# Kernel optimization log

Measured on AMD Instinct MI355X. Metric: run time of the kernel, lower is better.

Reference implementation:

```python
import jax, jax.numpy as jnp
import numpy as np

QK_C = 64
VX_C = 128

def conv1x1(x, W, b):
    # x: [B,C,H,W], W: [O,C], b: [O] -> [B,O,H,W]
    return jnp.einsum('bchw,oc->bohw', x, W) + b[None, :, None, None]

def setup_inputs() -> dict:
    key = jax.random.key(0)
    ks = jax.random.split(key, 9)
    B, H, W = 4, 64, 64
    x = jax.random.normal(ks[0], (B, QK_C, H, W), dtype=jnp.float32)
    x_h = jax.random.normal(ks[1], (B, VX_C, H, W), dtype=jnp.float32)
    qc = QK_C // 4
    s_qk = 1.0 / np.sqrt(QK_C)
    s_v = 1.0 / np.sqrt(VX_C)
    Wq = jax.random.normal(ks[2], (qc, QK_C), dtype=jnp.float32) * s_qk
    bq = jax.random.normal(ks[3], (qc,), dtype=jnp.float32) * 0.01
    Wk = jax.random.normal(ks[4], (qc, QK_C), dtype=jnp.float32) * s_qk
    bk = jax.random.normal(ks[5], (qc,), dtype=jnp.float32) * 0.01
    Wv = jax.random.normal(ks[6], (VX_C, VX_C), dtype=jnp.float32) * s_v
    bv = jax.random.normal(ks[7], (VX_C,), dtype=jnp.float32) * 0.01
    # gamma initialized to zero in the torch module; use a small nonzero value
    # so the attention branch actually contributes to the output/gradients.
    gamma = jnp.array([0.1], dtype=jnp.float32)
    return {"x": x, "x_h": x_h, "Wq": Wq, "bq": bq, "Wk": Wk, "bk": bk,
            "Wv": Wv, "bv": bv, "gamma": gamma}

def reference(x, x_h, Wq, bq, Wk, bk, Wv, bv, gamma):
    B, C, H, W = x_h.shape
    b, c, h, w = x.shape
    N = h * w
    # 1x1-conv projections, flattened over spatial positions
    q = conv1x1(x, Wq, bq).reshape(b, -1, N)          # [B, qc, N]
    k = conv1x1(x, Wk, bk).reshape(b, -1, N)          # [B, qc, N]
    v = conv1x1(x_h, Wv, bv).reshape(B, C, H * W)     # [B, C, N]
    # energy[b, i, j] = <q[:, i], k[:, j]>
    energy = jnp.einsum('bdi,bdj->bij', q, k)          # [B, N, N]
    attention = jax.nn.softmax(energy, axis=-1)
    # out[b, c, i] = sum_j v[b, c, j] * attention[b, i, j]
    out = jnp.einsum('bcj,bij->bci', v, attention)     # [B, C, N]
    out = out.reshape(B, C, H, W)
    return gamma[0] * out + x_h
```

## Files before the change

### kernel.cpp

```cpp
#include <hip/hip_runtime.h>

#define BB 4
#define NN 4096
#define CQK 64
#define DQ 16
#define CV 128

typedef __attribute__((ext_vector_type(8))) short bf16x8;
typedef __attribute__((ext_vector_type(4))) float f32x4;
typedef __attribute__((ext_vector_type(16))) float f32x16;
typedef __attribute__((ext_vector_type(8))) unsigned short u16x8;
typedef __attribute__((ext_vector_type(4))) unsigned int u32x4;

__device__ __forceinline__ unsigned short f2bf(float f) {
    unsigned int u = __builtin_bit_cast(unsigned int, f);
    u += 0x7FFFu + ((u >> 16) & 1u);
    return (unsigned short)(u >> 16);
}
__device__ __forceinline__ unsigned int pk_trunc(float lo, float hi) {
    unsigned int a = __builtin_bit_cast(unsigned int, lo);
    unsigned int b = __builtin_bit_cast(unsigned int, hi);
    return (a >> 16) | (b & 0xFFFF0000u);
}

__global__ __launch_bounds__(256, 4) void proj(
    const float* __restrict__ x,
    const float* __restrict__ Wq, const float* __restrict__ bq,
    const float* __restrict__ Wk, const float* __restrict__ bk,
    const float* __restrict__ xh,
    const float* __restrict__ Wv, const float* __restrict__ bv,
    unsigned short* __restrict__ qT, unsigned short* __restrict__ kT,
    unsigned short* __restrict__ vB)
{
    __shared__ __align__(16) float smem[8448];
    int tid = threadIdx.x;
    if (blockIdx.x >= 64) {
        float* wvT = smem;
        float* xs  = smem + 4224;
        float* bvs = smem + 8320;
        int bid = blockIdx.x - 64;
        int pt = bid >> 1, h = bid & 1;
        int i0 = pt * 64;
        int b = i0 >> 12, ib = i0 & 4095;
        int co0 = h * 64;
        if (tid < 64) bvs[tid] = bv[co0 + tid];
        int cog = tid & 31, ig = tid >> 5;
        float acc[8][2];
#pragma unroll
        for (int q = 0; q < 8; q++) { acc[q][0] = 0.f; acc[q][1] = 0.f; }

        for (int ch = 0; ch < 2; ch++) {
            for (int t = tid; t < 4096; t += 256) {
                int c = t & 63, col = t >> 6;
                wvT[c * 66 + col] = Wv[(size_t)(co0 + col) * CV + ch * 64 + c];
            }
            for (int t = tid; t < 4096; t += 256) {
                int il = t & 63, c = t >> 6;
                xs[c * 64 + il] = xh[((size_t)b * CV + ch * 64 + c) * NN + ib + il];
            }
            __syncthreads();
            for (int c = 0; c < 64; c++) {
                float2 w2 = *(const float2*)&wvT[c * 66 + cog * 2];
                float4 xa = *(const float4*)&xs[c * 64 + ig * 8];
                float4 xb = *(const float4*)&xs[c * 64 + ig * 8 + 4];
                float xv[8] = { xa.x, xa.y, xa.z, xa.w, xb.x, xb.y, xb.z, xb.w };
#pragma unroll
                for (int q = 0; q < 8; q++) {
                    acc[q][0] += xv[q] * w2.x;
                    acc[q][1] += xv[q] * w2.y;
                }
            }
            __syncthreads();
        }
        int kt = ib >> 6;
        int hb = ig & 1, kc = ig >> 1;
#pragma unroll
        for (int cc = 0; cc < 2; cc++) {
            int co = co0 + cog * 2 + cc;
            int g = co >> 5, cl = co & 31;
            float bb = bvs[cog * 2 + cc];
            u16x8 o;
#pragma unroll
            for (int jj = 0; jj < 8; jj++) o[jj] = f2bf(acc[jj][cc] + bb);
            size_t base = ((size_t)(b * 64 + kt)) * 8192
                        + (size_t)(((g * 4 + kc) * 64 + hb * 32 + cl)) * 8;
            *(u16x8*)(vB + base) = o;
        }
    } else {
        float* wqT = smem;
        float* wkT = smem + 1024;
        float* bqs = smem + 2048;
        float* bks = smem + 2064;
        for (int t = tid; t < 1024; t += 256) {
            int c = t & 63, d = t >> 6;
            wqT[c * 16 + d] = Wq[d * CQK + c];
            wkT[c * 16 + d] = Wk[d * CQK + c];
        }
        if (tid < DQ) { bqs[tid] = bq[tid]; bks[tid] = bk[tid]; }
        __syncthreads();

        int gidx = blockIdx.x * 256 + tid;
        int b = gidx >> 12, i = gidx & 4095;
        float qa[DQ], ka[DQ];
#pragma unroll
        for (int d = 0; d < DQ; d++) { qa[d] = bqs[d]; ka[d] = bks[d]; }
        const float* xp = x + (size_t)b * CQK * NN + i;
        for (int c = 0; c < CQK; c++) {
            float xv = xp[(size_t)c * NN];
            const float4* wq4 = (const float4*)&wqT[c * DQ];
            const float4* wk4 = (const float4*)&wkT[c * DQ];
#pragma unroll
            for (int dd = 0; dd < 4; dd++) {
                float4 a = wq4[dd], e = wk4[dd];
                qa[dd*4+0] += a.x * xv; qa[dd*4+1] += a.y * xv;
                qa[dd*4+2] += a.z * xv; qa[dd*4+3] += a.w * xv;
                ka[dd*4+0] += e.x * xv; ka[dd*4+1] += e.y * xv;
                ka[dd*4+2] += e.z * xv; ka[dd*4+3] += e.w * xv;
            }
        }
        u16x8 q0, q1, k0, k1;
#pragma unroll
        for (int dd = 0; dd < 8; dd++) {
            q0[dd] = f2bf(qa[dd]);     q1[dd] = f2bf(qa[8 + dd]);
            k0[dd] = f2bf(ka[dd]);     k1[dd] = f2bf(ka[8 + dd]);
        }
        u16x8* qo = (u16x8*)(qT + (size_t)gidx * DQ);
        u16x8* ko = (u16x8*)(kT + (size_t)gidx * DQ);
        qo[0] = q0; qo[1] = q1;
        ko[0] = k0; ko[1] = k1;
    }
}

__global__ __launch_bounds__(256, 2) void flash_mfma(
    const unsigned short* __restrict__ qTb,
    const unsigned short* __restrict__ kTb,
    const unsigned short* __restrict__ vB,
    const float* __restrict__ xh,
    const float* __restrict__ gamma,
    float* __restrict__ out)
{
    __shared__ __align__(16) float accs[32 * 132];
    __shared__ float l_s[4 * 2 * 32];

    int tid = threadIdx.x;
    int w = tid >> 6, lane = tid & 63;
    int q32 = lane & 31, half = lane >> 5;
    int b = blockIdx.x >> 7;
    int i0 = (blockIdx.x & 127) * 32;
    f32x16 zf16;
#pragma unroll
    for (int r = 0; r < 16; r++) zf16[r] = 0.f;

    bf16x8 qa = *(const bf16x8*)(qTb + ((size_t)(b * NN + i0 + q32)) * DQ + half * 8);

    f32x16 acc[4];
#pragma unroll
    for (int g = 0; g < 4; g++) acc[g] = zf16;
    float l = 0.f;

    const unsigned short* vtile = vB + ((size_t)(b * 64 + w * 16)) * 8192;
    const unsigned short* kbase = kTb + ((size_t)(b * NN + w * 16 * 64)) * DQ;

    bf16x8 kb[2], vb[16];
#pragma unroll
    for (int mg = 0; mg < 2; mg++)
        kb[mg] = *(const bf16x8*)(kbase + (size_t)(mg * 32 + q32) * DQ + half * 8);
#pragma unroll
    for (int i = 0; i < 16; i++)
        vb[i] = *(const bf16x8*)(vtile + (size_t)i * 512 + (size_t)lane * 8);

    for (int t = 0; t < 16; t++) {
        f32x16 s[2];
        s[0] = __builtin_amdgcn_mfma_f32_32x32x16_bf16(kb[0], qa, zf16, 0, 0, 0);
        s[1] = __builtin_amdgcn_mfma_f32_32x32x16_bf16(kb[1], qa, zf16, 0, 0, 0);
        const unsigned short* ktn = kbase + (size_t)(((t + 1) & 15) * 64) * DQ;
#pragma unroll
        for (int mg = 0; mg < 2; mg++)
            kb[mg] = *(const bf16x8*)(ktn + (size_t)(mg * 32 + q32) * DQ + half * 8);

        const unsigned short* vtn = vtile + ((t < 15) ? 8192 : 0);
#pragma unroll
        for (int u = 0; u < 4; u++) {
            const int mg = u >> 1, h8 = (u & 1) * 8;
            float p0 = __expf(s[mg][h8 + 0]);
            float p1 = __expf(s[mg][h8 + 1]);
            float p2 = __expf(s[mg][h8 + 2]);
            float p3 = __expf(s[mg][h8 + 3]);
            float p4 = __expf(s[mg][h8 + 4]);
            float p5 = __expf(s[mg][h8 + 5]);
            float p6 = __expf(s[mg][h8 + 6]);
            float p7 = __expf(s[mg][h8 + 7]);
            l += ((p0 + p1) + (p2 + p3)) + ((p4 + p5) + (p6 + p7));
            unsigned int A0 = pk_trunc(p0, p1), A1 = pk_trunc(p2, p3);
            unsigned int A2 = pk_trunc(p4, p5), A3 = pk_trunc(p6, p7);
            asm("v_permlane32_swap_b32 %0, %1" : "+v"(A0), "+v"(A2));
            asm("v_permlane32_swap_b32 %0, %1" : "+v"(A1), "+v"(A3));
            u32x4 pbw = { A0, A1, A2, A3 };
            bf16x8 pb = __builtin_bit_cast(bf16x8, pbw);
#pragma unroll
            for (int g = 0; g < 4; g++)
                acc[g] = __builtin_amdgcn_mfma_f32_32x32x16_bf16(vb[g * 4 + u], pb, acc[g], 0, 0, 0);
#pragma unroll
            for (int g = 0; g < 4; g++)
                vb[g * 4 + u] = *(const bf16x8*)(vtn + (size_t)(g * 4 + u) * 512 + (size_t)lane * 8);
        }
        vtile = vtn;
    }

    l_s[(w * 2 + half) * 32 + q32] = l;
    for (int ww = 0; ww < 4; ww++) {
        if (w == ww) {
#pragma unroll
            for (int g = 0; g < 4; g++)
#pragma unroll
                for (int r = 0; r < 4; r++) {
                    float* p = accs + q32 * 132 + g * 32 + r * 8 + half * 4;
                    f32x4 v4 = { acc[g][r*4+0], acc[g][r*4+1], acc[g][r*4+2], acc[g][r*4+3] };
                    if (ww == 0) *(f32x4*)p = v4;
                    else { f32x4 o = *(const f32x4*)p; *(f32x4*)p = o + v4; }
                }
        }
        __syncthreads();
    }

    float gam = gamma[0];
    int q = tid & 31, cg = tid >> 5;
    float L = 0.f;
#pragma unroll
    for (int u = 0; u < 8; u++) L += l_s[u * 32 + q];
    float linv = 1.f / L;
#pragma unroll
    for (int cc = 0; cc < 16; cc++) {
        int c = cg * 16 + cc;
        size_t gi = ((size_t)(b * CV + c)) * NN + i0 + q;
        out[gi] = gam * accs[q * 132 + c] * linv + xh[gi];
    }
}

extern "C" void kernel_launch(void* const* d_in, const int* in_sizes, int n_in,
                              void* d_out, int out_size, void* d_ws, size_t ws_size,
                              hipStream_t stream)
{
    (void)in_sizes; (void)n_in; (void)out_size; (void)ws_size;
    const float* x  = (const float*)d_in[0];
    const float* xh = (const float*)d_in[1];
    const float* Wq = (const float*)d_in[2];
    const float* bq = (const float*)d_in[3];
    const float* Wk = (const float*)d_in[4];
    const float* bk = (const float*)d_in[5];
    const float* Wv = (const float*)d_in[6];
    const float* bv = (const float*)d_in[7];
    const float* gm = (const float*)d_in[8];
    float* out = (float*)d_out;

    char* ws = (char*)d_ws;
    unsigned short* qTb = (unsigned short*)ws;
    unsigned short* kTb = (unsigned short*)(ws + (512 << 10));
    unsigned short* vB  = (unsigned short*)(ws + (1 << 20));

    proj<<<576, 256, 0, stream>>>(x, Wq, bq, Wk, bk, xh, Wv, bv, qTb, kTb, vB);
    flash_mfma<<<BB * 128, 256, 0, stream>>>(qTb, kTb, vB, xh, gm, out);
}
```

Before: 121.3 us.

## Process 64 queries per block with 8 waves sharing V fragments across two query tiles

Each block now handles 64 queries, split into two 32-query tiles, with 512 threads. Each of the 8 waves covers 8 key tiles, and every loaded V fragment feeds MFMAs for both query tiles, which halves V traffic per query. V loads are double-buffered through smaller register sets, and s_setprio is raised around the PV MFMAs. The cross-wave reduction now writes bf16 partials to LDS with one barrier instead of serialized f32 accumulation. This adds bf16 rounding of the partial outputs and uses more LDS, which may lower occupancy.

```diff
diff --git a/kernel.cpp b/kernel.cpp
--- a/kernel.cpp
+++ b/kernel.cpp
@@ -16,6 +16,12 @@
     unsigned int u = __builtin_bit_cast(unsigned int, f);
     u += 0x7FFFu + ((u >> 16) & 1u);
     return (unsigned short)(u >> 16);
+}
+__device__ __forceinline__ unsigned int pk2bf(float a, float b) {
+    return (unsigned int)f2bf(a) | ((unsigned int)f2bf(b) << 16);
+}
+__device__ __forceinline__ float bf2f(unsigned short u) {
+    return __builtin_bit_cast(float, (unsigned int)u << 16);
 }
 __device__ __forceinline__ unsigned int pk_trunc(float lo, float hi) {
     unsigned int a = __builtin_bit_cast(unsigned int, lo);
@@ -131,7 +137,7 @@
     }
 }
 
-__global__ __launch_bounds__(256, 2) void flash_mfma(
+__global__ __launch_bounds__(512, 2) void flash_mfma(
     const unsigned short* __restrict__ qTb,
     const unsigned short* __restrict__ kTb,
     const unsigned short* __restrict__ vB,
@@ -139,101 +145,136 @@
     const float* __restrict__ gamma,
     float* __restrict__ out)
 {
-    __shared__ __align__(16) float accs[32 * 132];
-    __shared__ float l_s[4 * 2 * 32];
+    __shared__ __align__(16) unsigned short part[8 * 64 * 132];
+    __shared__ float l_s[16 * 64];
 
     int tid = threadIdx.x;
     int w = tid >> 6, lane = tid & 63;
     int q32 = lane & 31, half = lane >> 5;
-    int b = blockIdx.x >> 7;
-    int i0 = (blockIdx.x & 127) * 32;
+    int p = blockIdx.x;
+    int b = (p >> 1) & 3;
+    int qg = ((p >> 3) << 1) | (p & 1);
+    int i0 = qg * 64;
     f32x16 zf16;
 #pragma unroll
     for (int r = 0; r < 16; r++) zf16[r] = 0.f;
 
-    bf16x8 qa = *(const bf16x8*)(qTb + ((size_t)(b * NN + i0 + q32)) * DQ + half * 8);
-
-    f32x16 acc[4];
-#pragma unroll
-    for (int g = 0; g < 4; g++) acc[g] = zf16;
-    float l = 0.f;
-
-    const unsigned short* vtile = vB + ((size_t)(b * 64 + w * 16)) * 8192;
-    const unsigned short* kbase = kTb + ((size_t)(b * NN + w * 16 * 64)) * DQ;
-
-    bf16x8 kb[2], vb[16];
+    bf16x8 qaA = *(const bf16x8*)(qTb + ((size_t)(b * NN + i0 + q32)) * DQ + half * 8);
+    bf16x8 qaB = *(const bf16x8*)(qTb + ((size_t)(b * NN + i0 + 32 + q32)) * DQ + half * 8);
+
+    f32x16 accA[4], accB[4];
+#pragma unroll
+    for (int g = 0; g < 4; g++) { accA[g] = zf16; accB[g] = zf16; }
+    float lA = 0.f, lB = 0.f;
+
+    const unsigned short* vtile = vB + ((size_t)(b * 64 + w * 8)) * 8192;
+    const unsigned short* kbase = kTb + ((size_t)(b * NN + w * 8 * 64)) * DQ;
+
+    bf16x8 kb[2], vc0[4], vc1[4];
 #pragma unroll
     for (int mg = 0; mg < 2; mg++)
         kb[mg] = *(const bf16x8*)(kbase + (size_t)(mg * 32 + q32) * DQ + half * 8);
 #pragma unroll
-    for (int i = 0; i < 16; i++)
-        vb[i] = *(const bf16x8*)(vtile + (size_t)i * 512 + (size_t)lane * 8);
-
-    for (int t = 0; t < 16; t++) {
-        f32x16 s[2];
-        s[0] = __builtin_amdgcn_mfma_f32_32x32x16_bf16(kb[0], qa, zf16, 0, 0, 0);
-        s[1] = __builtin_amdgcn_mfma_f32_32x32x16_bf16(kb[1], qa, zf16, 0, 0, 0);
-        const unsigned short* ktn = kbase + (size_t)(((t + 1) & 15) * 64) * DQ;
+    for (int g = 0; g < 4; g++)
+        vc0[g] = *(const bf16x8*)(vtile + (size_t)(g * 4) * 512 + (size_t)lane * 8);
+
+#define PACK_GRP(S0, S1, P, LACC)                                            \
+    _Pragma("unroll")                                                        \
+    for (int u = 0; u < 4; u++) {                                            \
+        const f32x16& sv = (u >> 1) ? (S1) : (S0);                           \
+        const int h8 = (u & 1) * 8;                                          \
+        float p0 = __expf(sv[h8 + 0]), p1 = __expf(sv[h8 + 1]);              \
+        float p2 = __expf(sv[h8 + 2]), p3 = __expf(sv[h8 + 3]);              \
+        float p4 = __expf(sv[h8 + 4]), p5 = __expf(sv[h8 + 5]);              \
+        float p6 = __expf(sv[h8 + 6]), p7 = __expf(sv[h8 + 7]);              \
+        LACC += ((p0 + p1) + (p2 + p3)) + ((p4 + p5) + (p6 + p7));           \
+        unsigned int A0 = pk_trunc(p0, p1), A1 = pk_trunc(p2, p3);           \
+        unsigned int A2 = pk_trunc(p4, p5), A3 = pk_trunc(p6, p7);           \
+        asm("v_permlane32_swap_b32 %0, %1" : "+v"(A0), "+v"(A2));            \
+        asm("v_permlane32_swap_b32 %0, %1" : "+v"(A1), "+v"(A3));            \
+        P[u] = (u32x4){A0, A1, A2, A3};                                      \
+    }
+
+#define PV_STEP(VCUR, VNXT, U)                                               \
+    {                                                                        \
+        const unsigned short* src = ((U) < 3) ? vtile : vtn;                 \
+        const int uu = ((U) + 1) & 3;                                        \
+        _Pragma("unroll")                                                    \
+        for (int g = 0; g < 4; g++)                                          \
+            VNXT[g] = *(const bf16x8*)(src + (size_t)(g * 4 + uu) * 512      \
+                                           + (size_t)lane * 8);              \
+        bf16x8 pa = __builtin_bit_cast(bf16x8, pA[U]);                       \
+        bf16x8 pbv = __builtin_bit_cast(bf16x8, pB[U]);                      \
+        __builtin_amdgcn_s_setprio(1);                                       \
+        _Pragma("unroll")                                                    \
+        for (int g = 0; g < 4; g++) {                                        \
+            accA[g] = __builtin_amdgcn_mfma_f32_32x32x16_bf16(VCUR[g], pa, accA[g], 0, 0, 0);  \
+            accB[g] = __builtin_amdgcn_mfma_f32_32x32x16_bf16(VCUR[g], pbv, accB[g], 0, 0, 0); \
+        }                                                                    \
+        __builtin_amdgcn_s_setprio(0);                                       \
+    }
+
+    for (int t = 0; t < 8; t++) {
+        f32x16 sA0 = __builtin_amdgcn_mfma_f32_32x32x16_bf16(kb[0], qaA, zf16, 0, 0, 0);
+        f32x16 sA1 = __builtin_amdgcn_mfma_f32_32x32x16_bf16(kb[1], qaA, zf16, 0, 0, 0);
+        u32x4 pA[4];
+        PACK_GRP(sA0, sA1, pA, lA)
+        f32x16 sB0 = __builtin_amdgcn_mfma_f32_32x32x16_bf16(kb[0], qaB, zf16, 0, 0, 0);
+        f32x16 sB1 = __builtin_amdgcn_mfma_f32_32x32x16_bf16(kb[1], qaB, zf16, 0, 0, 0);
+        const unsigned short* ktn = kbase + (size_t)(((t + 1) & 7) * 64) * DQ;
 #pragma unroll
         for (int mg = 0; mg < 2; mg++)
             kb[mg] = *(const bf16x8*)(ktn + (size_t)(mg * 32 + q32) * DQ + half * 8);
-
-        const unsigned short* vtn = vtile + ((t < 15) ? 8192 : 0);
-#pragma unroll
-        for (int u = 0; u < 4; u++) {
-            const int mg = u >> 1, h8 = (u & 1) * 8;
-            float p0 = __expf(s[mg][h8 + 0]);
-            float p1 = __expf(s[mg][h8 + 1]);
-            float p2 = __expf(s[mg][h8 + 2]);
-            float p3 = __expf(s[mg][h8 + 3]);
-            float p4 = __expf(s[mg][h8 + 4]);
-            float p5 = __expf(s[mg][h8 + 5]);
-            float p6 = __expf(s[mg][h8 + 6]);
-            float p7 = __expf(s[mg][h8 + 7]);
-            l += ((p0 + p1) + (p2 + p3)) + ((p4 + p5) + (p6 + p7));
-            unsigned int A0 = pk_trunc(p0, p1), A1 = pk_trunc(p2, p3);
-            unsigned int A2 = pk_trunc(p4, p5), A3 = pk_trunc(p6, p7);
-            asm("v_permlane32_swap_b32 %0, %1" : "+v"(A0), "+v"(A2));
-            asm("v_permlane32_swap_b32 %0, %1" : "+v"(A1), "+v"(A3));
-            u32x4 pbw = { A0, A1, A2, A3 };
-            bf16x8 pb = __builtin_bit_cast(bf16x8, pbw);
-#pragma unroll
-            for (int g = 0; g < 4; g++)
-                acc[g] = __builtin_amdgcn_mfma_f32_32x32x16_bf16(vb[g * 4 + u], pb, acc[g], 0, 0, 0);
-#pragma unroll
-            for (int g = 0; g < 4; g++)
-                vb[g * 4 + u] = *(const bf16x8*)(vtn + (size_t)(g * 4 + u) * 512 + (size_t)lane * 8);
-        }
+        u32x4 pB[4];
+        PACK_GRP(sB0, sB1, pB, lB)
+
+        const unsigned short* vtn = vtile + ((t < 7) ? 8192 : 0);
+        PV_STEP(vc0, vc1, 0)
+        PV_STEP(vc1, vc0, 1)
+        PV_STEP(vc0, vc1, 2)
+        PV_STEP(vc1, vc0, 3)
         vtile = vtn;
     }
 
-    l_s[(w * 2 + half) * 32 + q32] = l;
-    for (int ww = 0; ww < 4; ww++) {
-        if (w == ww) {
-#pragma unroll
-            for (int g = 0; g < 4; g++)
-#pragma unroll
-                for (int r = 0; r < 4; r++) {
-                    float* p = accs + q32 * 132 + g * 32 + r * 8 + half * 4;
-                    f32x4 v4 = { acc[g][r*4+0], acc[g][r*4+1], acc[g][r*4+2], acc[g][r*4+3] };
-                    if (ww == 0) *(f32x4*)p = v4;
-                    else { f32x4 o = *(const f32x4*)p; *(f32x4*)p = o + v4; }
-                }
-        }
-        __syncthreads();
-    }
+    l_s[(w * 2 + half) * 64 + q32] = lA;
+    l_s[(w * 2 + half) * 64 + 32 + q32] = lB;
+    unsigned short* pw = part + (size_t)w * (64 * 132);
+#pragma unroll
+    for (int g = 0; g < 4; g++)
+#pragma unroll
+        for (int r = 0; r < 4; r++) {
+            int colb = g * 32 + r * 8 + half * 4;
+            uint2 da = { pk2bf(accA[g][r * 4 + 0], accA[g][r * 4 + 1]),
+                         pk2bf(accA[g][r * 4 + 2], accA[g][r * 4 + 3]) };
+            uint2 db = { pk2bf(accB[g][r * 4 + 0], accB[g][r * 4 + 1]),
+                         pk2bf(accB[g][r * 4 + 2], accB[g][r * 4 + 3]) };
+            *(uint2*)(pw + q32 * 132 + colb) = da;
+            *(uint2*)(pw + (32 + q32) * 132 + colb) = db;
+        }
+    __syncthreads();
 
     float gam = gamma[0];
-    int q = tid & 31, cg = tid >> 5;
+    int q = tid & 63, cg = tid >> 6;
     float L = 0.f;
 #pragma unroll
-    for (int u = 0; u < 8; u++) L += l_s[u * 32 + q];
+    for (int e = 0; e < 16; e++) L += l_s[e * 64 + q];
     float linv = 1.f / L;
+    float o[16];
+#pragma unroll
+    for (int cc = 0; cc < 16; cc++) o[cc] = 0.f;
+#pragma unroll
+    for (int e = 0; e < 8; e++) {
+        const unsigned short* pr = part + (size_t)e * (64 * 132) + q * 132 + cg * 16;
+        u16x8 v0 = *(const u16x8*)pr;
+        u16x8 v1 = *(const u16x8*)(pr + 8);
+#pragma unroll
+        for (int j = 0; j < 8; j++) { o[j] += bf2f(v0[j]); o[8 + j] += bf2f(v1[j]); }
+    }
 #pragma unroll
     for (int cc = 0; cc < 16; cc++) {
         int c = cg * 16 + cc;
         size_t gi = ((size_t)(b * CV + c)) * NN + i0 + q;
-        out[gi] = gam * accs[q * 132 + c] * linv + xh[gi];
+        out[gi] = gam * o[cc] * linv + xh[gi];
     }
 }
 
@@ -259,5 +300,5 @@
     unsigned short* vB  = (unsigned short*)(ws + (1 << 20));
 
     proj<<<576, 256, 0, stream>>>(x, Wq, bq, Wk, bk, xh, Wv, bv, qTb, kTb, vB);
-    flash_mfma<<<BB * 128, 256, 0, stream>>>(qTb, kTb, vB, xh, gm, out);
-}
+    flash_mfma<<<BB * 64, 512, 0, stream>>>(qTb, kTb, vB, xh, gm, out);
+}
```

After: 159.8 us. +31.7%, slower.

## Compute V projection with bf16 MFMA directly from global memory

Applied to the files above, without the earlier changes.

The V 1x1-conv projection moves from a scalar FP32 FMA loop over LDS-staged tiles to 32x32x16 bf16 MFMA instructions. Each block now handles a 64-position tile across all 128 output channels, so the grid shrinks and LDS use drops. Operands are read straight from global memory and truncated to bf16. Results are repacked with permlane32 swaps to match the existing vB layout. This cuts projection compute time but adds bf16 truncation error on the V inputs and weights, and relies on uncoalesced strided loads.

```diff
diff --git a/kernel.cpp b/kernel.cpp
--- a/kernel.cpp
+++ b/kernel.cpp
@@ -16,6 +16,9 @@
     unsigned int u = __builtin_bit_cast(unsigned int, f);
     u += 0x7FFFu + ((u >> 16) & 1u);
     return (unsigned short)(u >> 16);
+}
+__device__ __forceinline__ unsigned int pk2bf(float a, float b) {
+    return (unsigned int)f2bf(a) | ((unsigned int)f2bf(b) << 16);
 }
 __device__ __forceinline__ unsigned int pk_trunc(float lo, float hi) {
     unsigned int a = __builtin_bit_cast(unsigned int, lo);
@@ -32,60 +35,69 @@
     unsigned short* __restrict__ qT, unsigned short* __restrict__ kT,
     unsigned short* __restrict__ vB)
 {
-    __shared__ __align__(16) float smem[8448];
+    __shared__ __align__(16) float smem[2112];
     int tid = threadIdx.x;
     if (blockIdx.x >= 64) {
-        float* wvT = smem;
-        float* xs  = smem + 4224;
-        float* bvs = smem + 8320;
         int bid = blockIdx.x - 64;
-        int pt = bid >> 1, h = bid & 1;
-        int i0 = pt * 64;
-        int b = i0 >> 12, ib = i0 & 4095;
-        int co0 = h * 64;
-        if (tid < 64) bvs[tid] = bv[co0 + tid];
-        int cog = tid & 31, ig = tid >> 5;
-        float acc[8][2];
-#pragma unroll
-        for (int q = 0; q < 8; q++) { acc[q][0] = 0.f; acc[q][1] = 0.f; }
-
-        for (int ch = 0; ch < 2; ch++) {
-            for (int t = tid; t < 4096; t += 256) {
-                int c = t & 63, col = t >> 6;
-                wvT[c * 66 + col] = Wv[(size_t)(co0 + col) * CV + ch * 64 + c];
-            }
-            for (int t = tid; t < 4096; t += 256) {
-                int il = t & 63, c = t >> 6;
-                xs[c * 64 + il] = xh[((size_t)b * CV + ch * 64 + c) * NN + ib + il];
-            }
-            __syncthreads();
-            for (int c = 0; c < 64; c++) {
-                float2 w2 = *(const float2*)&wvT[c * 66 + cog * 2];
-                float4 xa = *(const float4*)&xs[c * 64 + ig * 8];
-                float4 xb = *(const float4*)&xs[c * 64 + ig * 8 + 4];
-                float xv[8] = { xa.x, xa.y, xa.z, xa.w, xb.x, xb.y, xb.z, xb.w };
-#pragma unroll
-                for (int q = 0; q < 8; q++) {
-                    acc[q][0] += xv[q] * w2.x;
-                    acc[q][1] += xv[q] * w2.y;
-                }
-            }
-            __syncthreads();
-        }
-        int kt = ib >> 6;
-        int hb = ig & 1, kc = ig >> 1;
-#pragma unroll
-        for (int cc = 0; cc < 2; cc++) {
-            int co = co0 + cog * 2 + cc;
-            int g = co >> 5, cl = co & 31;
-            float bb = bvs[cog * 2 + cc];
-            u16x8 o;
-#pragma unroll
-            for (int jj = 0; jj < 8; jj++) o[jj] = f2bf(acc[jj][cc] + bb);
-            size_t base = ((size_t)(b * 64 + kt)) * 8192
-                        + (size_t)(((g * 4 + kc) * 64 + hb * 32 + cl)) * 8;
-            *(u16x8*)(vB + base) = o;
-        }
+        int b = bid >> 6, kt = bid & 63;
+        int lane = tid & 63, w = tid >> 6;
+        int pt = w & 1, gh = w >> 1;
+        int cl = lane & 31, kh = lane >> 5;
+        int pos = kt * 64 + pt * 32 + cl;
+        const float* xb = xh + (size_t)b * CV * NN;
+        f32x16 zf16;
+#pragma unroll
+        for (int r = 0; r < 16; r++) zf16[r] = 0.f;
+        f32x16 c0 = zf16, c1 = zf16;
+        float bv0 = bv[(gh * 2 + 0) * 32 + cl];
+        float bv1 = bv[(gh * 2 + 1) * 32 + cl];
+
+#pragma unroll
+        for (int kc = 0; kc < 8; ++kc) {
+            int cin0 = kc * 16 + kh * 8;
+            const float* xc = xb + (size_t)cin0 * NN + pos;
+            float f0 = xc[0 * NN], f1 = xc[1 * NN], f2 = xc[2 * NN], f3 = xc[3 * NN];
+            float f4 = xc[4 * NN], f5 = xc[5 * NN], f6 = xc[6 * NN], f7 = xc[7 * NN];
+            u32x4 aw = { pk_trunc(f0, f1), pk_trunc(f2, f3),
+                         pk_trunc(f4, f5), pk_trunc(f6, f7) };
+            bf16x8 af = __builtin_bit_cast(bf16x8, aw);
+            const float* wp0 = Wv + (size_t)((gh * 2 + 0) * 32 + cl) * CV + cin0;
+            float4 wa = *(const float4*)wp0, wb_ = *(const float4*)(wp0 + 4);
+            u32x4 bw0 = { pk_trunc(wa.x, wa.y), pk_trunc(wa.z, wa.w),
+                          pk_trunc(wb_.x, wb_.y), pk_trunc(wb_.z, wb_.w) };
+            const float* wp1 = Wv + (size_t)((gh * 2 + 1) * 32 + cl) * CV + cin0;
+            float4 wc = *(const float4*)wp1, wd = *(const float4*)(wp1 + 4);
+            u32x4 bw1 = { pk_trunc(wc.x, wc.y), pk_trunc(wc.z, wc.w),
+                          pk_trunc(wd.x, wd.y), pk_trunc(wd.z, wd.w) };
+            c0 = __builtin_amdgcn_mfma_f32_32x32x16_bf16(
+                     af, __builtin_bit_cast(bf16x8, bw0), c0, 0, 0, 0);
+            c1 = __builtin_amdgcn_mfma_f32_32x32x16_bf16(
+                     af, __builtin_bit_cast(bf16x8, bw1), c1, 0, 0, 0);
+        }
+
+        size_t tb = (size_t)(b * 64 + kt) * 8192;
+#define EMIT_G(CVEC, G, BVV)                                                 \
+        {                                                                    \
+            unsigned int A0 = pk2bf(CVEC[0] + BVV, CVEC[1] + BVV);           \
+            unsigned int A1 = pk2bf(CVEC[2] + BVV, CVEC[3] + BVV);           \
+            unsigned int A2 = pk2bf(CVEC[4] + BVV, CVEC[5] + BVV);           \
+            unsigned int A3 = pk2bf(CVEC[6] + BVV, CVEC[7] + BVV);           \
+            asm("v_permlane32_swap_b32 %0, %1" : "+v"(A0), "+v"(A2));        \
+            asm("v_permlane32_swap_b32 %0, %1" : "+v"(A1), "+v"(A3));        \
+            *(u32x4*)(vB + tb + (size_t)((G) * 4 + pt * 2) * 512             \
+                         + (size_t)lane * 8) = (u32x4){A0, A1, A2, A3};      \
+            unsigned int B0 = pk2bf(CVEC[8] + BVV, CVEC[9] + BVV);           \
+            unsigned int B1 = pk2bf(CVEC[10] + BVV, CVEC[11] + BVV);         \
+            unsigned int B2 = pk2bf(CVEC[12] + BVV, CVEC[13] + BVV);         \
+            unsigned int B3 = pk2bf(CVEC[14] + BVV, CVEC[15] + BVV);         \
+            asm("v_permlane32_swap_b32 %0, %1" : "+v"(B0), "+v"(B2));        \
+            asm("v_permlane32_swap_b32 %0, %1" : "+v"(B1), "+v"(B3));        \
+            *(u32x4*)(vB + tb + (size_t)((G) * 4 + pt * 2 + 1) * 512         \
+                         + (size_t)lane * 8) = (u32x4){B0, B1, B2, B3};      \
+        }
+        EMIT_G(c0, gh * 2 + 0, bv0)
+        EMIT_G(c1, gh * 2 + 1, bv1)
+#undef EMIT_G
     } else {
         float* wqT = smem;
         float* wkT = smem + 1024;
@@ -258,6 +270,6 @@
     unsigned short* kTb = (unsigned short*)(ws + (512 << 10));
     unsigned short* vB  = (unsigned short*)(ws + (1 << 20));
 
-    proj<<<576, 256, 0, stream>>>(x, Wq, bq, Wk, bk, xh, Wv, bv, qTb, kTb, vB);
+    proj<<<320, 256, 0, stream>>>(x, Wq, bq, Wk, bk, xh, Wv, bv, qTb, kTb, vB);
     flash_mfma<<<BB * 128, 256, 0, stream>>>(qTb, kTb, vB, xh, gm, out);
 }
```

New measurement: 129.8 us. +6.9%, slower.

## Software-pipeline softmax exp with PV MFMA, fold log2e into Q, reorder blocks

Applied to the files above, without the earlier changes.

The attention loop is restructured so the exponentials and bf16 packing of the score tile for iteration t run after the PV MFMAs of iteration t-1. That lets the MFMA pipe overlap with the VALU exp work, and a prologue and epilogue handle the edges. The log2(e) factor is folded into Q during projection so the hot loop can use raw exp2, and s_setprio raises wave priority around the MFMA block. Block indices are also interleaved across batches. These changes cost extra registers for the packed P tiles and duplicate some loop code.

```diff
diff --git a/kernel.cpp b/kernel.cpp
--- a/kernel.cpp
+++ b/kernel.cpp
@@ -118,11 +118,12 @@
                 ka[dd*4+2] += e.z * xv; ka[dd*4+3] += e.w * xv;
             }
         }
+        const float L2E = 1.44269504088896f;
         u16x8 q0, q1, k0, k1;
 #pragma unroll
         for (int dd = 0; dd < 8; dd++) {
-            q0[dd] = f2bf(qa[dd]);     q1[dd] = f2bf(qa[8 + dd]);
-            k0[dd] = f2bf(ka[dd]);     k1[dd] = f2bf(ka[8 + dd]);
+            q0[dd] = f2bf(qa[dd] * L2E);  q1[dd] = f2bf(qa[8 + dd] * L2E);
+            k0[dd] = f2bf(ka[dd]);        k1[dd] = f2bf(ka[8 + dd]);
         }
         u16x8* qo = (u16x8*)(qT + (size_t)gidx * DQ);
         u16x8* ko = (u16x8*)(kT + (size_t)gidx * DQ);
@@ -145,8 +146,9 @@
     int tid = threadIdx.x;
     int w = tid >> 6, lane = tid & 63;
     int q32 = lane & 31, half = lane >> 5;
-    int b = blockIdx.x >> 7;
-    int i0 = (blockIdx.x & 127) * 32;
+    int p = blockIdx.x;
+    int b = p & 3;
+    int i0 = (p >> 2) * 32;
     f32x16 zf16;
 #pragma unroll
     for (int r = 0; r < 16; r++) zf16[r] = 0.f;
@@ -169,34 +171,49 @@
     for (int i = 0; i < 16; i++)
         vb[i] = *(const bf16x8*)(vtile + (size_t)i * 512 + (size_t)lane * 8);
 
-    for (int t = 0; t < 16; t++) {
-        f32x16 s[2];
-        s[0] = __builtin_amdgcn_mfma_f32_32x32x16_bf16(kb[0], qa, zf16, 0, 0, 0);
-        s[1] = __builtin_amdgcn_mfma_f32_32x32x16_bf16(kb[1], qa, zf16, 0, 0, 0);
-        const unsigned short* ktn = kbase + (size_t)(((t + 1) & 15) * 64) * DQ;
+#define PACK_U(SV, U)                                                        \
+    {                                                                        \
+        const int h8 = ((U) & 1) * 8;                                        \
+        float e0 = __builtin_amdgcn_exp2f(SV[h8 + 0]);                       \
+        float e1 = __builtin_amdgcn_exp2f(SV[h8 + 1]);                       \
+        float e2 = __builtin_amdgcn_exp2f(SV[h8 + 2]);                       \
+        float e3 = __builtin_amdgcn_exp2f(SV[h8 + 3]);                       \
+        float e4 = __builtin_amdgcn_exp2f(SV[h8 + 4]);                       \
+        float e5 = __builtin_amdgcn_exp2f(SV[h8 + 5]);                       \
+        float e6 = __builtin_amdgcn_exp2f(SV[h8 + 6]);                       \
+        float e7 = __builtin_amdgcn_exp2f(SV[h8 + 7]);                       \
+        l += ((e0 + e1) + (e2 + e3)) + ((e4 + e5) + (e6 + e7));              \
+        unsigned int A0 = pk_trunc(e0, e1), A1 = pk_trunc(e2, e3);           \
+        unsigned int A2 = pk_trunc(e4, e5), A3 = pk_trunc(e6, e7);           \
+        asm("v_permlane32_swap_b32 %0, %1" : "+v"(A0), "+v"(A2));            \
+        asm("v_permlane32_swap_b32 %0, %1" : "+v"(A1), "+v"(A3));            \
+        pbs[U] = (u32x4){A0, A1, A2, A3};                                    \
+    }
+
+    u32x4 pbs[4];
+    {
+        f32x16 sa = __builtin_amdgcn_mfma_f32_32x32x16_bf16(kb[0], qa, zf16, 0, 0, 0);
+        f32x16 sb = __builtin_amdgcn_mfma_f32_32x32x16_bf16(kb[1], qa, zf16, 0, 0, 0);
+        const unsigned short* ktn = kbase + (size_t)64 * DQ;
 #pragma unroll
         for (int mg = 0; mg < 2; mg++)
             kb[mg] = *(const bf16x8*)(ktn + (size_t)(mg * 32 + q32) * DQ + half * 8);
-
-        const unsigned short* vtn = vtile + ((t < 15) ? 8192 : 0);
+        PACK_U(sa, 0) PACK_U(sa, 1) PACK_U(sb, 2) PACK_U(sb, 3)
+    }
+
+    for (int t = 1; t < 16; t++) {
+        f32x16 sa = __builtin_amdgcn_mfma_f32_32x32x16_bf16(kb[0], qa, zf16, 0, 0, 0);
+        f32x16 sb = __builtin_amdgcn_mfma_f32_32x32x16_bf16(kb[1], qa, zf16, 0, 0, 0);
+        const unsigned short* ktn = kbase + (size_t)(((t + 1) & 15) * 64) * DQ;
+#pragma unroll
+        for (int mg = 0; mg < 2; mg++)
+            kb[mg] = *(const bf16x8*)(ktn + (size_t)(mg * 32 + q32) * DQ + half * 8);
+
+        const unsigned short* vtn = vtile + 8192;
+        __builtin_amdgcn_s_setprio(1);
 #pragma unroll
         for (int u = 0; u < 4; u++) {
-            const int mg = u >> 1, h8 = (u & 1) * 8;
-            float p0 = __expf(s[mg][h8 + 0]);
-            float p1 = __expf(s[mg][h8 + 1]);
-            float p2 = __expf(s[mg][h8 + 2]);
-            float p3 = __expf(s[mg][h8 + 3]);
-            float p4 = __expf(s[mg][h8 + 4]);
-            float p5 = __expf(s[mg][h8 + 5]);
-            float p6 = __expf(s[mg][h8 + 6]);
-            float p7 = __expf(s[mg][h8 + 7]);
-            l += ((p0 + p1) + (p2 + p3)) + ((p4 + p5) + (p6 + p7));
-            unsigned int A0 = pk_trunc(p0, p1), A1 = pk_trunc(p2, p3);
-            unsigned int A2 = pk_trunc(p4, p5), A3 = pk_trunc(p6, p7);
-            asm("v_permlane32_swap_b32 %0, %1" : "+v"(A0), "+v"(A2));
-            asm("v_permlane32_swap_b32 %0, %1" : "+v"(A1), "+v"(A3));
-            u32x4 pbw = { A0, A1, A2, A3 };
-            bf16x8 pb = __builtin_bit_cast(bf16x8, pbw);
+            bf16x8 pb = __builtin_bit_cast(bf16x8, pbs[u]);
 #pragma unroll
             for (int g = 0; g < 4; g++)
                 acc[g] = __builtin_amdgcn_mfma_f32_32x32x16_bf16(vb[g * 4 + u], pb, acc[g], 0, 0, 0);
@@ -204,8 +221,20 @@
             for (int g = 0; g < 4; g++)
                 vb[g * 4 + u] = *(const bf16x8*)(vtn + (size_t)(g * 4 + u) * 512 + (size_t)lane * 8);
         }
+        __builtin_amdgcn_s_setprio(0);
         vtile = vtn;
-    }
+
+        PACK_U(sa, 0) PACK_U(sa, 1) PACK_U(sb, 2) PACK_U(sb, 3)
+    }
+
+#pragma unroll
+    for (int u = 0; u < 4; u++) {
+        bf16x8 pb = __builtin_bit_cast(bf16x8, pbs[u]);
+#pragma unroll
+        for (int g = 0; g < 4; g++)
+            acc[g] = __builtin_amdgcn_mfma_f32_32x32x16_bf16(vb[g * 4 + u], pb, acc[g], 0, 0, 0);
+    }
+#undef PACK_U
 
     l_s[(w * 2 + half) * 32 + q32] = l;
     for (int ww = 0; ww < 4; ww++) {
@@ -214,10 +243,10 @@
             for (int g = 0; g < 4; g++)
 #pragma unroll
                 for (int r = 0; r < 4; r++) {
-                    float* p = accs + q32 * 132 + g * 32 + r * 8 + half * 4;
+                    float* pp = accs + q32 * 132 + g * 32 + r * 8 + half * 4;
                     f32x4 v4 = { acc[g][r*4+0], acc[g][r*4+1], acc[g][r*4+2], acc[g][r*4+3] };
-                    if (ww == 0) *(f32x4*)p = v4;
-                    else { f32x4 o = *(const f32x4*)p; *(f32x4*)p = o + v4; }
+                    if (ww == 0) *(f32x4*)pp = v4;
+                    else { f32x4 o = *(const f32x4*)pp; *(f32x4*)pp = o + v4; }
                 }
         }
         __syncthreads();
```

Measured after the change: 125.1 us. +3.1%, slower.
